# Kernel optimization log

Hardware: AMD Instinct MI355X
Metric: run time of the kernel (lower is better)

## Reference

```python
import jax, jax.numpy as jnp
import numpy as np

B, P, S, FX, D, DFF, OUT = 8, 10, 160, 11, 64, 256, 1


def _layernorm(h, g, b, eps=1e-6):
    mu = jnp.mean(h, axis=-1, keepdims=True)
    var = jnp.mean(jnp.square(h - mu), axis=-1, keepdims=True)
    return g * (h - mu) * jax.lax.rsqrt(var + eps) + b


def setup_inputs() -> dict:
    key = jax.random.key(0)
    ks = jax.random.split(key, 16)
    n = lambda k, shp, s=0.05: (jax.random.normal(k, shp, jnp.float32) * s)
    return {
        "inputs": jax.random.normal(ks[0], (B, P, S, FX), jnp.float32),
        "targets": jax.random.normal(ks[1], (B, P, S, OUT), jnp.float32),
        "W_proj": n(ks[2], (FX, D)), "b_proj": jnp.zeros((D,), jnp.float32),
        "Wq": n(ks[3], (D, D)), "bq": jnp.zeros((D,), jnp.float32),
        "Wk": n(ks[4], (D, D)), "bk": jnp.zeros((D,), jnp.float32),
        "Wv": n(ks[5], (D, D)), "bv": jnp.zeros((D,), jnp.float32),
        "Wo": n(ks[6], (D, D)), "bo": jnp.zeros((D,), jnp.float32),
        "ln1_g": jnp.ones((D,), jnp.float32), "ln1_b": jnp.zeros((D,), jnp.float32),
        "W1": n(ks[7], (D, DFF)), "b1": jnp.zeros((DFF,), jnp.float32),
        "W2": n(ks[8], (DFF, D)), "b2": jnp.zeros((D,), jnp.float32),
        "ln2_g": jnp.ones((D,), jnp.float32), "ln2_b": jnp.zeros((D,), jnp.float32),
        "Wf": n(ks[9], (D, OUT)), "bf": jnp.zeros((OUT,), jnp.float32),
    }


def reference(inputs, targets, W_proj, b_proj, Wq, bq, Wk, bk, Wv, bv, Wo, bo,
              ln1_g, ln1_b, W1, b1, W2, b2, ln2_g, ln2_b, Wf, bf):
    # inputs: (B,P,S,FX); no-noise (inference/deterministic) SMC-Transformer path:
    # K/V/R resampling is identity, so R_resampl == R.
    d_model = W_proj.shape[1]
    s_len = inputs.shape[2]
    x = (inputs @ W_proj + b_proj) * jnp.sqrt(jnp.float32(d_model))  # (B,P,S,D)
    scale = 1.0 / jnp.sqrt(jnp.float32(d_model))
    pos = jnp.arange(s_len)
    K0 = jnp.zeros(x.shape, jnp.float32)

    def step(carry, inp_t):
        K, V, R = carry
        xt, t = inp_t                                  # xt: (B,P,D), t: scalar
        q = xt @ Wq + bq
        k = xt @ Wk + bk
        v = xt @ Wv + bv
        K = jax.lax.dynamic_update_slice(K, k[:, :, None, :], (0, 0, t, 0))
        V = jax.lax.dynamic_update_slice(V, v[:, :, None, :], (0, 0, t, 0))
        logits = jnp.einsum('bpd,bpsd->bps', q, K) * scale
        logits = jnp.where(pos <= t, logits, jnp.float32(-1e9))  # causal mask
        attn = jax.nn.softmax(logits, axis=-1)                   # (B,P,S)
        z = jnp.einsum('bps,bpsd->bpd', attn, V) @ Wo + bo
        out = _layernorm(z + xt, ln1_g, ln1_b)
        r = jax.nn.relu(out @ W1 + b1) @ W2 + b2                 # pointwise FFN
        r = _layernorm(r + out, ln2_g, ln2_b)
        R = jax.lax.dynamic_update_slice(R, r[:, :, None, :], (0, 0, t, 0))
        return (K, V, R), (r, attn)

    xs = (jnp.transpose(x, (2, 0, 1, 3)), jnp.arange(s_len))
    (K, V, R), (rs, attns) = jax.lax.scan(step, (K0, K0, K0), xs)
    R_out = jnp.transpose(rs, (1, 2, 0, 3))        # (B,P,S,D)
    attn_weights = jnp.transpose(attns, (1, 2, 0, 3))  # (B,P,S,S)
    pred = R_out @ Wf + bf
    pred_resampl = R @ Wf + bf
    return (pred, pred_resampl, K, V, R, attn_weights)
```

## Files before the change

### kernel.cpp

```cpp
#include <hip/hip_runtime.h>
#include <math.h>

#define BB 8
#define PP 10
#define SS 160
#define FXD 11
#define DD 64
#define DFF 256
#define NROW (BB*PP*SS)
#define NBP  (BB*PP)

#define OFF_PRED  0
#define OFF_PREDR 12800
#define OFF_K     25600
#define OFF_V     844800
#define OFF_R     1664000
#define OFF_ATTN  2483200

typedef short short8 __attribute__((ext_vector_type(8)));
typedef float f32x4  __attribute__((ext_vector_type(4)));

__device__ __forceinline__ void fma4(float4& acc, float s, const float4& b){
  acc.x += s*b.x; acc.y += s*b.y; acc.z += s*b.z; acc.w += s*b.w;
}
template<int N>
__device__ __forceinline__ void wred_sum_n(float (&v)[N]){
#pragma unroll
  for (int m = 32; m >= 1; m >>= 1){
#pragma unroll
    for (int i = 0; i < N; ++i) v[i] += __shfl_xor(v[i], m, 64);
  }
}
template<int N>
__device__ __forceinline__ void qred_sum_n(float (&v)[N]){
#pragma unroll
  for (int m = 8; m >= 1; m >>= 1){
#pragma unroll
    for (int i = 0; i < N; ++i) v[i] += __shfl_xor(v[i], m, 64);
  }
}
template<int N>
__device__ __forceinline__ void qred_max_n(float (&v)[N]){
#pragma unroll
  for (int m = 8; m >= 1; m >>= 1){
#pragma unroll
    for (int i = 0; i < N; ++i) v[i] = fmaxf(v[i], __shfl_xor(v[i], m, 64));
  }
}
__device__ __forceinline__ unsigned f2bf(float f){
  unsigned u = __float_as_uint(f);
  return (u + 0x7fffu + ((u >> 16) & 1u)) >> 16;
}
__device__ __forceinline__ unsigned packbf2(float x, float y){
  return f2bf(x) | (f2bf(y) << 16);
}
__device__ __forceinline__ f32x4 mfma16(uint4 a, uint4 b, f32x4 c){
  union { uint4 u; short8 s; } ua, ub;
  ua.u = a; ub.u = b;
  return __builtin_amdgcn_mfma_f32_16x16x32_bf16(ua.s, ub.s, c, 0, 0, 0);
}
__device__ __forceinline__ uint4 pack8(float4 a, float4 b){
  uint4 r;
  r.x = packbf2(a.x, a.y); r.y = packbf2(a.z, a.w);
  r.z = packbf2(b.x, b.y); r.w = packbf2(b.z, b.w);
  return r;
}

__global__ __launch_bounds__(256) void k_xqkv(const float* __restrict__ inp,
    const float* __restrict__ Wp, const float* __restrict__ bpj,
    const float* __restrict__ Wq, const float* __restrict__ bq,
    const float* __restrict__ Wk, const float* __restrict__ bk,
    const float* __restrict__ Wv, const float* __restrict__ bv,
    const float* __restrict__ Wo, const float* __restrict__ W1,
    const float* __restrict__ W2, unsigned* __restrict__ wpack,
    float* __restrict__ x, float* __restrict__ Q,
    float* __restrict__ Kc, float* __restrict__ Vc){
  __shared__ __align__(16) float ins[16*12];
  __shared__ __align__(16) unsigned xs2[16*36];
  int tid = threadIdx.x;
  int g = blockIdx.x;
  int row0 = g*16;
  {
    int pi = g*256 + tid;
    if (pi < 18432){
      const float* W; int N, K2, base, off;
      if (pi < 2048){ W = Wo; N = 64; K2 = 32; base = 0; off = pi; }
      else if (pi < 10240){ W = W1; N = 256; K2 = 32; base = 2048; off = pi - 2048; }
      else { W = W2; N = 64; K2 = 128; base = 10240; off = pi - 10240; }
      int n = off % N, k2 = off / N;
      wpack[base + n*K2 + k2] = packbf2(W[(2*k2)*N + n], W[(2*k2+1)*N + n]);
    }
  }
  for (int i = tid; i < 16*FXD; i += 256){
    int r = i / FXD, f = i - r*FXD;
    ins[r*12 + f] = inp[row0*FXD + i];
  }
  __syncthreads();
  int tc = tid & 15, tr = tid >> 4;
  {
    float4 a = make_float4(0.f,0.f,0.f,0.f);
#pragma unroll
    for (int f = 0; f < FXD; ++f){
      float v = ins[tr*12 + f];
      float4 w4 = *(const float4*)&Wp[f*64 + tc*4];
      fma4(a, v, w4);
    }
    float4 bp4 = *(const float4*)&bpj[tc*4];
    float4 xv = make_float4((a.x+bp4.x)*8.f, (a.y+bp4.y)*8.f,
                            (a.z+bp4.z)*8.f, (a.w+bp4.w)*8.f);
    *(float4*)&x[(row0+tr)*64 + tc*4] = xv;
    xs2[tr*36 + tc*2]     = packbf2(xv.x, xv.y);
    xs2[tr*36 + tc*2 + 1] = packbf2(xv.z, xv.w);
  }
  __syncthreads();
  int lane = tid & 63, w = tid >> 6, nl = lane & 15, q = lane >> 4;
  uint4 a0 = *(const uint4*)&xs2[nl*36 + q*4];
  uint4 a1 = *(const uint4*)&xs2[nl*36 + 16 + q*4];
  int n = w*16 + nl;
  const float* Wm[3] = {Wq, Wk, Wv};
  const float* bias[3] = {bq, bk, bv};
  float* Out[3] = {Q, Kc, Vc};
#pragma unroll
  for (int mat = 0; mat < 3; ++mat){
    const float* W = Wm[mat];
    float w0 = W[(q*8+0)*64+n], w1 = W[(q*8+1)*64+n];
    float w2 = W[(q*8+2)*64+n], w3 = W[(q*8+3)*64+n];
    float w4 = W[(q*8+4)*64+n], w5 = W[(q*8+5)*64+n];
    float w6 = W[(q*8+6)*64+n], w7 = W[(q*8+7)*64+n];
    uint4 b0; b0.x = packbf2(w0,w1); b0.y = packbf2(w2,w3);
    b0.z = packbf2(w4,w5); b0.w = packbf2(w6,w7);
    float v0 = W[(32+q*8+0)*64+n], v1 = W[(32+q*8+1)*64+n];
    float v2 = W[(32+q*8+2)*64+n], v3 = W[(32+q*8+3)*64+n];
    float v4 = W[(32+q*8+4)*64+n], v5 = W[(32+q*8+5)*64+n];
    float v6 = W[(32+q*8+6)*64+n], v7 = W[(32+q*8+7)*64+n];
    uint4 b1; b1.x = packbf2(v0,v1); b1.y = packbf2(v2,v3);
    b1.z = packbf2(v4,v5); b1.w = packbf2(v6,v7);
    f32x4 acc = {0.f,0.f,0.f,0.f};
    acc = mfma16(a0, b0, acc);
    acc = mfma16(a1, b1, acc);
    float bvv = bias[mat][n];
    float* O = Out[mat];
#pragma unroll
    for (int r = 0; r < 4; ++r)
      O[(row0 + q*4 + r)*64 + n] = acc[r] + bvv;
  }
}

__global__ __launch_bounds__(256, 4) void k_attn_ffn(const float* __restrict__ Qg,
    const float* __restrict__ Kout, const float* __restrict__ Vout,
    const unsigned* __restrict__ wpack,
    const float* __restrict__ bo,
    const float* __restrict__ g1, const float* __restrict__ b1l,
    const float* __restrict__ x,
    const float* __restrict__ b1, const float* __restrict__ b2,
    const float* __restrict__ g2, const float* __restrict__ b2l,
    const float* __restrict__ Wf, const float* __restrict__ bf,
    float* __restrict__ attn, float* __restrict__ R,
    float* __restrict__ pred, float* __restrict__ predr){
  __shared__ __align__(16) unsigned char smA[5376];
  unsigned* ps2 = (unsigned*)smA;
  float*    zos = (float*)smA;
  __shared__ float mws[80], sws[80];
  __shared__ __align__(16) float zs[16*68];
  __shared__ __align__(16) float os[16*68];
  __shared__ __align__(16) unsigned os2[16*36];
  __shared__ __align__(16) unsigned as2[16*132];
  __shared__ __align__(16) float lnb[16*68];

  int tid = threadIdx.x;
  int bp = blockIdx.x, c = blockIdx.y;
  int t0 = c*16;
  const float* Kb = Kout + bp*(SS*DD);
  const float* Vb = Vout + bp*(SS*DD);
  const float* Qb = Qg + bp*(SS*DD);
  float* Ab = attn + bp*(SS*SS);
  const unsigned* wop = wpack;
  const unsigned* w1p = wpack + 2048;
  const unsigned* w2p = wpack + 10240;

  int lane = tid & 63, w = tid >> 6, nl = lane & 15, q = lane >> 4;

  int ntiles = (w < 2) ? 3 : 2;
  {
    const float* qr = &Qb[(t0+nl)*64];
    uint4 aq0 = pack8(*(const float4*)&qr[q*8],    *(const float4*)&qr[q*8+4]);
    uint4 aq1 = pack8(*(const float4*)&qr[32+q*8], *(const float4*)&qr[32+q*8+4]);
    float lg[3][4], ev[3][4];
    f32x4 pacc[3];
#pragma unroll
    for (int i = 0; i < 3; ++i){
      pacc[i] = (f32x4){0.f,0.f,0.f,0.f};
      if (i < ntiles){
        const float* kr = &Kb[((w+4*i)*16 + nl)*64];
        uint4 b0 = pack8(*(const float4*)&kr[q*8],    *(const float4*)&kr[q*8+4]);
        uint4 b1 = pack8(*(const float4*)&kr[32+q*8], *(const float4*)&kr[32+q*8+4]);
        pacc[i] = mfma16(aq0, b0, pacc[i]);
        pacc[i] = mfma16(aq1, b1, pacc[i]);
      }
    }
    float mw_[4];
#pragma unroll
    for (int r = 0; r < 4; ++r){
      int t = t0 + q*4 + r;
      float m_ = -1e30f;
#pragma unroll
      for (int i = 0; i < 3; ++i){
        if (i < ntiles){
          int s = (w + 4*i)*16 + nl;
          float l = (s <= t) ? pacc[i][r]*0.125f : -1e30f;
          lg[i][r] = l; m_ = fmaxf(m_, l);
        }
      }
      mw_[r] = m_;
    }
    qred_max_n<4>(mw_);
    float sw_[4];
#pragma unroll
    for (int r = 0; r < 4; ++r){
      float s_ = 0.f;
#pragma unroll
      for (int i = 0; i < 3; ++i){
        if (i < ntiles){
          float e = __expf(lg[i][r] - mw_[r]);
          ev[i][r] = e; s_ += e;
        }
      }
      sw_[r] = s_;
    }
    qred_sum_n<4>(sw_);
    if (nl == 0){
#pragma unroll
      for (int r = 0; r < 4; ++r){
        mws[(q*4+r)*5 + w] = mw_[r];
        sws[(q*4+r)*5 + w] = sw_[r];
      }
    }
    __syncthreads();
    float scale[4];
#pragma unroll
    for (int r = 0; r < 4; ++r){
      int row = q*4 + r;
      float m0 = mws[row*5+0], m1 = mws[row*5+1];
      float m2 = mws[row*5+2], m3 = mws[row*5+3];
      float gm = fmaxf(fmaxf(m0,m1), fmaxf(m2,m3));
      float tot = sws[row*5+0]*__expf(m0-gm) + sws[row*5+1]*__expf(m1-gm)
                + sws[row*5+2]*__expf(m2-gm) + sws[row*5+3]*__expf(m3-gm);
      scale[r] = __expf(mw_[r]-gm) / tot;
    }
#pragma unroll
    for (int i = 0; i < 3; ++i){
      if (i < ntiles){
        int s = (w + 4*i)*16 + nl;
#pragma unroll
        for (int r = 0; r < 4; ++r){
          float p_ = ev[i][r] * scale[r];
          Ab[(t0 + q*4 + r)*SS + s] = p_;
          float pn = __shfl_xor(p_, 1, 64);
          if (!(nl & 1))
            ps2[(q*4+r)*84 + (w+4*i)*8 + (nl >> 1)] = packbf2(p_, pn);
        }
      }
    }
  }
  __syncthreads();

  {
    int d = w*16 + nl;
    f32x4 zacc = {0.f,0.f,0.f,0.f};
#pragma unroll
    for (int ks = 0; ks < 5; ++ks){
      int sb = ks*32 + q*8;
      uint4 bv;
      bv.x = packbf2(Vb[(sb+0)*64+d], Vb[(sb+1)*64+d]);
      bv.y = packbf2(Vb[(sb+2)*64+d], Vb[(sb+3)*64+d]);
      bv.z = packbf2(Vb[(sb+4)*64+d], Vb[(sb+5)*64+d]);
      bv.w = packbf2(Vb[(sb+6)*64+d], Vb[(sb+7)*64+d]);
      uint4 ap = *(const uint4*)&ps2[nl*84 + ks*16 + q*4];
      zacc = mfma16(ap, bv, zacc);
    }
#pragma unroll
    for (int r = 0; r < 4; ++r)
      zs[(q*4+r)*68 + d] = zacc[r];
  }
  __syncthreads();

  {
    f32x4 cacc = {0.f,0.f,0.f,0.f};
#pragma unroll
    for (int ks = 0; ks < 2; ++ks){
      float4 f0 = *(const float4*)&zs[nl*68 + ks*32 + q*8];
      float4 f1 = *(const float4*)&zs[nl*68 + ks*32 + q*8 + 4];
      uint4 a = pack8(f0, f1);
      uint4 b = *(const uint4*)&wop[(w*16+nl)*32 + ks*16 + q*4];
      cacc = mfma16(a, b, cacc);
    }
    int col = w*16 + nl;
    float bov = bo[col];
#pragma unroll
    for (int r = 0; r < 4; ++r){
      int row = q*4 + r;
      int grow = bp*SS + t0 + row;
      zos[row*68 + col] = cacc[r] + bov + x[grow*64 + col];
    }
  }
  __syncthreads();

  {
    float h[4], s8v[8];
#pragma unroll
    for (int j = 0; j < 4; ++j){
      int r = w + 4*j;
      h[j] = zos[r*68 + lane];
      s8v[j] = h[j]; s8v[4+j] = h[j]*h[j];
    }
    wred_sum_n<8>(s8v);
    float gl = g1[lane], bl = b1l[lane];
#pragma unroll
    for (int j = 0; j < 4; ++j){
      int r = w + 4*j;
      float mu = s8v[j]*(1.f/64.f);
      float var = s8v[4+j]*(1.f/64.f) - mu*mu;
      float o = gl*(h[j]-mu)*rsqrtf(fmaxf(var,0.f) + 1e-6f) + bl;
      os[r*68 + lane] = o;
      float on = __shfl_xor(o, 1, 64);
      if (!(lane & 1)) os2[r*36 + (lane >> 1)] = packbf2(o, on);
    }
  }
  __syncthreads();

  {
    uint4 ao0 = *(const uint4*)&os2[nl*36 + q*4];
    uint4 ao1 = *(const uint4*)&os2[nl*36 + 16 + q*4];
    f32x4 fa[4];
#pragma unroll
    for (int i = 0; i < 4; ++i){
      fa[i] = (f32x4){0.f,0.f,0.f,0.f};
      int n = (w*4+i)*16 + nl;
      uint4 b0 = *(const uint4*)&w1p[n*32 + q*4];
      uint4 b1v = *(const uint4*)&w1p[n*32 + 16 + q*4];
      fa[i] = mfma16(ao0, b0, fa[i]);
      fa[i] = mfma16(ao1, b1v, fa[i]);
    }
#pragma unroll
    for (int i = 0; i < 4; ++i){
      int n = (w*4+i)*16 + nl;
      float b1b = b1[n];
#pragma unroll
      for (int r = 0; r < 4; ++r){
        float a_ = fmaxf(fa[i][r] + b1b, 0.f);
        float an = __shfl_xor(a_, 1, 64);
        if (!(nl & 1))
          as2[(q*4+r)*132 + w*32 + i*8 + (nl >> 1)] = packbf2(a_, an);
      }
    }
  }
  __syncthreads();

  {
    f32x4 f2 = {0.f,0.f,0.f,0.f};
#pragma unroll
    for (int ks = 0; ks < 8; ++ks){
      uint4 a = *(const uint4*)&as2[nl*132 + ks*16 + q*4];
      uint4 b = *(const uint4*)&w2p[(w*16+nl)*128 + ks*16 + q*4];
      f2 = mfma16(a, b, f2);
    }
    int col = w*16 + nl;
    float b2v = b2[col];
#pragma unroll
    for (int r = 0; r < 4; ++r){
      int row = q*4 + r;
      lnb[row*68 + col] = f2[r] + b2v + os[row*68 + col];
    }
  }
  __syncthreads();

  {
    float wfv = Wf[lane], bfv = bf[0];
    float h[4], s8v[8];
#pragma unroll
    for (int j = 0; j < 4; ++j){
      int r = w*4 + j;
      h[j] = lnb[r*68 + lane];
      s8v[j] = h[j]; s8v[4+j] = h[j]*h[j];
    }
    wred_sum_n<8>(s8v);
    float g2l = g2[lane], b2ll = b2l[lane];
    float pr[4];
#pragma unroll
    for (int j = 0; j < 4; ++j){
      int r = w*4 + j;
      float mu = s8v[j]*(1.f/64.f);
      float var = s8v[4+j]*(1.f/64.f) - mu*mu;
      float rv = g2l*(h[j]-mu)*rsqrtf(fmaxf(var,0.f) + 1e-6f) + b2ll;
      int grow = bp*SS + t0 + r;
      R[grow*64 + lane] = rv;
      pr[j] = rv * wfv;
    }
    wred_sum_n<4>(pr);
    if (lane == 0){
#pragma unroll
      for (int j = 0; j < 4; ++j){
        int grow = bp*SS + t0 + w*4 + j;
        pred[grow]  = pr[j] + bfv;
        predr[grow] = pr[j] + bfv;
      }
    }
  }
}

extern "C" void kernel_launch(void* const* d_in, const int* in_sizes, int n_in,
                              void* d_out, int out_size, void* d_ws, size_t ws_size,
                              hipStream_t stream){
  const float* inputs = (const float*)d_in[0];
  const float* Wp  = (const float*)d_in[2];
  const float* bpj = (const float*)d_in[3];
  const float* Wq  = (const float*)d_in[4];  const float* bq  = (const float*)d_in[5];
  const float* Wk  = (const float*)d_in[6];  const float* bk  = (const float*)d_in[7];
  const float* Wv  = (const float*)d_in[8];  const float* bv  = (const float*)d_in[9];
  const float* Wo  = (const float*)d_in[10]; const float* bo  = (const float*)d_in[11];
  const float* g1  = (const float*)d_in[12]; const float* b1l = (const float*)d_in[13];
  const float* W1  = (const float*)d_in[14]; const float* b1  = (const float*)d_in[15];
  const float* W2  = (const float*)d_in[16]; const float* b2  = (const float*)d_in[17];
  const float* g2  = (const float*)d_in[18]; const float* b2l = (const float*)d_in[19];
  const float* Wf  = (const float*)d_in[20]; const float* bf  = (const float*)d_in[21];

  float* outp = (float*)d_out;
  float* ws   = (float*)d_ws;
  float* x    = ws;
  float* Qw   = ws + 819200;
  unsigned* wpack = (unsigned*)(ws + 1638400);

  float* pred  = outp + OFF_PRED;
  float* predr = outp + OFF_PREDR;
  float* Kc    = outp + OFF_K;
  float* Vc    = outp + OFF_V;
  float* Rr    = outp + OFF_R;
  float* attn  = outp + OFF_ATTN;

  k_xqkv<<<NROW/16, 256, 0, stream>>>(inputs, Wp, bpj, Wq, bq, Wk, bk, Wv, bv,
                                      Wo, W1, W2, wpack, x, Qw, Kc, Vc);
  k_attn_ffn<<<dim3(NBP, 10), 256, 0, stream>>>(Qw, Kc, Vc, wpack,
                                                bo, g1, b1l, x, b1, b2,
                                                g2, b2l, Wf, bf,
                                                attn, Rr, pred, predr);
}
```

Before: 131.6 us.

## Prepack Q/K/V as bf16 and skip causally masked attention tiles

```diff
diff --git a/kernel.cpp b/kernel.cpp
--- a/kernel.cpp
+++ b/kernel.cpp
@@ -73,7 +73,8 @@
     const float* __restrict__ Wv, const float* __restrict__ bv,
     const float* __restrict__ Wo, const float* __restrict__ W1,
     const float* __restrict__ W2, unsigned* __restrict__ wpack,
-    float* __restrict__ x, float* __restrict__ Q,
+    float* __restrict__ x, unsigned* __restrict__ Qp,
+    unsigned* __restrict__ Kp, unsigned* __restrict__ Vp,
     float* __restrict__ Kc, float* __restrict__ Vc){
   __shared__ __align__(16) float ins[16*12];
   __shared__ __align__(16) unsigned xs2[16*36];
@@ -117,9 +118,10 @@
   uint4 a0 = *(const uint4*)&xs2[nl*36 + q*4];
   uint4 a1 = *(const uint4*)&xs2[nl*36 + 16 + q*4];
   int n = w*16 + nl;
+  bool evenlane = !(lane & 1);
+  int bpg = g / 10, loc0 = (g - bpg*10)*16;
   const float* Wm[3] = {Wq, Wk, Wv};
   const float* bias[3] = {bq, bk, bv};
-  float* Out[3] = {Q, Kc, Vc};
 #pragma unroll
   for (int mat = 0; mat < 3; ++mat){
     const float* W = Wm[mat];
@@ -139,16 +141,36 @@
     acc = mfma16(a0, b0, acc);
     acc = mfma16(a1, b1, acc);
     float bvv = bias[mat][n];
-    float* O = Out[mat];
-#pragma unroll
-    for (int r = 0; r < 4; ++r)
-      O[(row0 + q*4 + r)*64 + n] = acc[r] + bvv;
-  }
-}
-
-__global__ __launch_bounds__(256, 4) void k_attn_ffn(const float* __restrict__ Qg,
-    const float* __restrict__ Kout, const float* __restrict__ Vout,
-    const unsigned* __restrict__ wpack,
+    float o[4];
+#pragma unroll
+    for (int r = 0; r < 4; ++r) o[r] = acc[r] + bvv;
+    if (mat == 0){
+#pragma unroll
+      for (int r = 0; r < 4; ++r){
+        float on = __shfl_xor(o[r], 1, 64);
+        if (evenlane) Qp[(row0 + q*4 + r)*32 + (n >> 1)] = packbf2(o[r], on);
+      }
+    } else if (mat == 1){
+#pragma unroll
+      for (int r = 0; r < 4; ++r){
+        Kc[(row0 + q*4 + r)*64 + n] = o[r];
+        float on = __shfl_xor(o[r], 1, 64);
+        if (evenlane) Kp[(row0 + q*4 + r)*32 + (n >> 1)] = packbf2(o[r], on);
+      }
+    } else {
+#pragma unroll
+      for (int r = 0; r < 4; ++r)
+        Vc[(row0 + q*4 + r)*64 + n] = o[r];
+      unsigned* vd = &Vp[bpg*(64*80) + n*80 + (loc0 >> 1) + q*2];
+      vd[0] = packbf2(o[0], o[1]);
+      vd[1] = packbf2(o[2], o[3]);
+    }
+  }
+}
+
+__global__ __launch_bounds__(256, 4) void k_attn_ffn(
+    const unsigned* __restrict__ Qp, const unsigned* __restrict__ Kp,
+    const unsigned* __restrict__ Vp, const unsigned* __restrict__ wpack,
     const float* __restrict__ bo,
     const float* __restrict__ g1, const float* __restrict__ b1l,
     const float* __restrict__ x,
@@ -170,9 +192,6 @@
   int tid = threadIdx.x;
   int bp = blockIdx.x, c = blockIdx.y;
   int t0 = c*16;
-  const float* Kb = Kout + bp*(SS*DD);
-  const float* Vb = Vout + bp*(SS*DD);
-  const float* Qb = Qg + bp*(SS*DD);
   float* Ab = attn + bp*(SS*SS);
   const unsigned* wop = wpack;
   const unsigned* w1p = wpack + 2048;
@@ -180,20 +199,35 @@
 
   int lane = tid & 63, w = tid >> 6, nl = lane & 15, q = lane >> 4;
 
-  int ntiles = (w < 2) ? 3 : 2;
-  {
-    const float* qr = &Qb[(t0+nl)*64];
-    uint4 aq0 = pack8(*(const float4*)&qr[q*8],    *(const float4*)&qr[q*8+4]);
-    uint4 aq1 = pack8(*(const float4*)&qr[32+q*8], *(const float4*)&qr[32+q*8+4]);
+  {
+    int zc0 = (c+1)*16;
+    int zcw = 160 - zc0;
+    int nq = (16*zcw) >> 2;
+    int perrow = zcw >> 2;
+    for (int i = tid; i < nq; i += 256){
+      int r = i / perrow, col = zc0 + (i - r*perrow)*4;
+      *(float4*)&Ab[(t0 + r)*SS + col] = make_float4(0.f,0.f,0.f,0.f);
+    }
+    if (!(c & 1) && tid < 128){
+      int r = tid >> 3, j = tid & 7;
+      ps2[r*84 + (c+1)*8 + j] = 0;
+    }
+  }
+
+  int ntiles = (w <= c) ? (((c - w) >> 2) + 1) : 0;
+  {
+    const unsigned* qpr = &Qp[(bp*SS + t0 + nl)*32];
+    uint4 aq0 = *(const uint4*)&qpr[q*4];
+    uint4 aq1 = *(const uint4*)&qpr[16 + q*4];
     float lg[3][4], ev[3][4];
     f32x4 pacc[3];
 #pragma unroll
     for (int i = 0; i < 3; ++i){
       pacc[i] = (f32x4){0.f,0.f,0.f,0.f};
       if (i < ntiles){
-        const float* kr = &Kb[((w+4*i)*16 + nl)*64];
-        uint4 b0 = pack8(*(const float4*)&kr[q*8],    *(const float4*)&kr[q*8+4]);
-        uint4 b1 = pack8(*(const float4*)&kr[32+q*8], *(const float4*)&kr[32+q*8+4]);
+        const unsigned* kpr = &Kp[(bp*SS + (w+4*i)*16 + nl)*32];
+        uint4 b0 = *(const uint4*)&kpr[q*4];
+        uint4 b1 = *(const uint4*)&kpr[16 + q*4];
         pacc[i] = mfma16(aq0, b0, pacc[i]);
         pacc[i] = mfma16(aq1, b1, pacc[i]);
       }
@@ -265,18 +299,17 @@
   __syncthreads();
 
   {
+    int nks = (c + 2) >> 1;
     int d = w*16 + nl;
+    const unsigned* vpd = &Vp[bp*(64*80) + d*80];
     f32x4 zacc = {0.f,0.f,0.f,0.f};
 #pragma unroll
     for (int ks = 0; ks < 5; ++ks){
-      int sb = ks*32 + q*8;
-      uint4 bv;
-      bv.x = packbf2(Vb[(sb+0)*64+d], Vb[(sb+1)*64+d]);
-      bv.y = packbf2(Vb[(sb+2)*64+d], Vb[(sb+3)*64+d]);
-      bv.z = packbf2(Vb[(sb+4)*64+d], Vb[(sb+5)*64+d]);
-      bv.w = packbf2(Vb[(sb+6)*64+d], Vb[(sb+7)*64+d]);
-      uint4 ap = *(const uint4*)&ps2[nl*84 + ks*16 + q*4];
-      zacc = mfma16(ap, bv, zacc);
+      if (ks < nks){
+        uint4 bv = *(const uint4*)&vpd[ks*16 + q*4];
+        uint4 ap = *(const uint4*)&ps2[nl*84 + ks*16 + q*4];
+        zacc = mfma16(ap, bv, zacc);
+      }
     }
 #pragma unroll
     for (int r = 0; r < 4; ++r)
@@ -427,8 +460,10 @@
   float* outp = (float*)d_out;
   float* ws   = (float*)d_ws;
   float* x    = ws;
-  float* Qw   = ws + 819200;
-  unsigned* wpack = (unsigned*)(ws + 1638400);
+  unsigned* Qp = (unsigned*)(ws + 819200);
+  unsigned* Kp = Qp + 409600;
+  unsigned* Vp = Kp + 409600;
+  unsigned* wpack = Vp + 409600;
 
   float* pred  = outp + OFF_PRED;
   float* predr = outp + OFF_PREDR;
@@ -438,8 +473,8 @@
   float* attn  = outp + OFF_ATTN;
 
   k_xqkv<<<NROW/16, 256, 0, stream>>>(inputs, Wp, bpj, Wq, bq, Wk, bk, Wv, bv,
-                                      Wo, W1, W2, wpack, x, Qw, Kc, Vc);
-  k_attn_ffn<<<dim3(NBP, 10), 256, 0, stream>>>(Qw, Kc, Vc, wpack,
+                                      Wo, W1, W2, wpack, x, Qp, Kp, Vp, Kc, Vc);
+  k_attn_ffn<<<dim3(NBP, 10), 256, 0, stream>>>(Qp, Kp, Vp, wpack,
                                                 bo, g1, b1l, x, b1, b2,
                                                 g2, b2l, Wf, bf,
                                                 attn, Rr, pred, predr);
```

Result: faster. 128.4 us (-2.4%).
